# Optimization experiments

Measured on AMD Instinct MI355X. Metric: run time of the kernel, lower is better.

## Reference

```python
import jax, jax.numpy as jnp
import numpy as np

B, N, L, E = 4, 8, 2048, 16384
CH = [128, 256, 256, 256]
EPS = 1e-5
USE_MAX = True


def setup_inputs() -> dict:
    key = jax.random.key(0)
    ks = jax.random.split(key, 10)
    d = {}
    d["x"] = jax.random.normal(ks[0], (B, N, CH[0], L), jnp.float32)
    d["edge_index"] = jax.random.randint(ks[1], (2, E), 0, L, dtype=jnp.int32)
    wspecs = [("W1", CH[0], CH[1]), ("W2", CH[1], CH[2]), ("W3", CH[2], CH[3]),
              ("W1s", CH[0], CH[1]), ("W2s", CH[1], CH[2]), ("W3s", CH[2], CH[3])]
    for i, (nm, ci, co) in enumerate(wspecs):
        std = (2.0 / (ci + co)) ** 0.5  # xavier_normal
        d[nm] = std * jax.random.normal(ks[2 + i], (ci, co), jnp.float32)
        d["b" + nm[1:]] = jnp.zeros((co,), jnp.float32)
    for nm, co in [("1", CH[1]), ("2", CH[2]), ("3", CH[3]),
                   ("1s", CH[1]), ("2s", CH[2]), ("3s", CH[3])]:
        d["g" + nm] = jnp.ones((co,), jnp.float32)
        d["be" + nm] = jnp.zeros((co,), jnp.float32)
    return d


def _gcn_norm(edge_index, num_nodes):
    # PyG gcn_norm with improved=True: A_hat = A + 2I, sym normalization.
    src, dst = edge_index[0], edge_index[1]
    loop = jnp.arange(num_nodes, dtype=src.dtype)
    src = jnp.concatenate([src, loop])
    dst = jnp.concatenate([dst, loop])
    w = jnp.concatenate([jnp.ones((edge_index.shape[1],), jnp.float32),
                         jnp.full((num_nodes,), 2.0, jnp.float32)])
    deg = jnp.zeros((num_nodes,), jnp.float32).at[dst].add(w)
    dis = jnp.where(deg > 0, jax.lax.rsqrt(deg), 0.0)
    return src, dst, dis[src] * w * dis[dst]


def _gcn(h, W, bias, src, dst, norm, num_nodes):
    # h: [G, L, Cin] node features for G independent copies of the shared graph
    hw = h @ W  # [G, L, Cout]
    msgs = hw[:, src, :] * norm[None, :, None]  # gather along nodes
    agg = jnp.zeros((h.shape[0], num_nodes, W.shape[1]), h.dtype).at[:, dst].add(msgs)
    return agg + bias


def _bn(x, g, be):
    # x: [Nb, C, L]; training-mode BatchNorm1d over (Nb, L) per channel
    m = x.mean(axis=(0, 2), keepdims=True)
    v = x.var(axis=(0, 2), keepdims=True)
    return g[None, :, None] * (x - m) * jax.lax.rsqrt(v + EPS) + be[None, :, None]


def _forward(x, edge_index, params):
    b, n, c, l = x.shape
    src, dst, norm = _gcn_norm(edge_index, l)
    xo = None
    for (W, bias, Ws, bs, g, be, gs, bes) in params:
        # per-element branch
        h = x.reshape(b * n, x.shape[2], l).transpose(0, 2, 1)  # [b*n, L, C]
        x1 = _gcn(h, W, bias, src, dst, norm, l).transpose(0, 2, 1)  # [b*n, Cout, L]
        x1 = _bn(x1, g, be)
        # symmetric pooled branch
        xp = jnp.max(x, axis=1) if USE_MAX else jnp.sum(x, axis=1)  # [b, C, L]
        x2 = _gcn(xp.transpose(0, 2, 1), Ws, bs, src, dst, norm, l).transpose(0, 2, 1)
        x2 = _bn(x2, gs, bes)
        co = x2.shape[1]
        x2 = jnp.broadcast_to(x2[:, None], (b, n, co, l)).reshape(b * n, co, l)
        xo = jax.nn.relu(x1 + x2)  # [b*n, Cout, L]
        x = xo.reshape(b, n, co, l)
    return xo  # final output is [b*n, CH[3], L] (not reshaped back)


def reference(x, edge_index, W1, b1, W2, b2, W3, b3, W1s, b1s, W2s, b2s, W3s, b3s,
              g1, be1, g2, be2, g3, be3, g1s, be1s, g2s, be2s, g3s, be3s):
    params = [(W1, b1, W1s, b1s, g1, be1, g1s, be1s),
              (W2, b2, W2s, b2s, g2, be2, g2s, be2s),
              (W3, b3, W3s, b3s, g3, be3, g3s, be3s)]
    return _forward(x, edge_index, params)
```

## Files before the change

### kernel.cpp

```cpp
#include <hip/hip_runtime.h>
#include <math.h>

#define LNODES 2048
#define NEDGE 16384
#define GBIG 32
#define GSM 4
#define NCOUT 256
#define BN_EPS 1e-5f
#define ND 32

typedef unsigned short u16;
typedef __attribute__((ext_vector_type(8))) short bf16x8;
typedef __attribute__((ext_vector_type(4))) float f32x4;

__device__ __forceinline__ unsigned pk2(float a, float b) {
  unsigned ua = __float_as_uint(a); ua += 0x7fffu + ((ua >> 16) & 1u);
  unsigned ub = __float_as_uint(b); ub += 0x7fffu + ((ub >> 16) & 1u);
  return (ua >> 16) | (ub & 0xffff0000u);
}
__device__ __forceinline__ float blo(unsigned u) { return __uint_as_float(u << 16); }
__device__ __forceinline__ float bhi(unsigned u) { return __uint_as_float(u & 0xffff0000u); }

__device__ __forceinline__ void gl16(const u16* g, u16* l) {
  __builtin_amdgcn_global_load_lds(
      (const __attribute__((address_space(1))) void*)g,
      (__attribute__((address_space(3))) void*)l, 16, 0, 0);
}


struct WCvt {
  const float* src[6];
  u16* dst[6];
  int ci[6];
};

__global__ __launch_bounds__(256) void setup1_k(const int* __restrict__ ei,
                                                float* __restrict__ deg,
                                                int* __restrict__ cnt,
                                                WCvt wp,
                                                const float* __restrict__ x_in,
                                                u16* __restrict__ XT0) {
  __shared__ float T[64][65];
  const int bid = blockIdx.x;
  const int t = threadIdx.x;
  if (bid < 64) {
    int e = bid * 256 + t;
    int d = ei[NEDGE + e];
    atomicAdd(&deg[d], 1.0f);
    atomicAdd(&cnt[d], 1);
  } else if (bid < 160) {
    const int w = bid - 64;
    const int bz = w >> 4;
    const int Ci = wp.ci[bz];
    const int ci0 = ((w >> 2) & 3) * 64;
    if (ci0 >= Ci) return;
    const float* W = wp.src[bz];
    u16* WT = wp.dst[bz];
    const int co0 = (w & 3) * 64;
    const int tr = t >> 4;
    const int tc = (t & 15) * 4;
#pragma unroll
    for (int p = 0; p < 4; ++p) {
      int ci = ci0 + tr + p * 16;
      float4 v = *reinterpret_cast<const float4*>(&W[(size_t)ci * NCOUT + co0 + tc]);
      T[tr + p * 16][tc + 0] = v.x; T[tr + p * 16][tc + 1] = v.y;
      T[tr + p * 16][tc + 2] = v.z; T[tr + p * 16][tc + 3] = v.w;
    }
    __syncthreads();
    const int ci = ci0 + tc;
    const int kt = ci >> 5;
    const int kk = ci & 31;
#pragma unroll
    for (int p = 0; p < 4; ++p) {
      int co = co0 + tr + p * 16;
      uint2 o = {pk2(T[tc + 0][co - co0], T[tc + 1][co - co0]),
                 pk2(T[tc + 2][co - co0], T[tc + 3][co - co0])};
      size_t idx = (size_t)kt * 8192 + (unsigned)((co * 32 + kk) ^ ((co & 7) << 3));
      *reinterpret_cast<uint2*>(&WT[idx]) = o;
    }
  } else {
    const int w = bid - 160;
    const int g = w >> 6;
    const int n0 = (w & 31) * 64;
    const int c0 = ((w >> 5) & 1) * 64;
    const int tr = t >> 4;
    const int tc = (t & 15) * 4;
#pragma unroll
    for (int p = 0; p < 4; ++p) {
      int ci = c0 + tr + p * 16;
      float4 v = *reinterpret_cast<const float4*>(&x_in[((size_t)g * 128 + ci) * LNODES + n0 + tc]);
      T[tr + p * 16][tc + 0] = v.x; T[tr + p * 16][tc + 1] = v.y;
      T[tr + p * 16][tc + 2] = v.z; T[tr + p * 16][tc + 3] = v.w;
    }
    __syncthreads();
#pragma unroll
    for (int p = 0; p < 4; ++p) {
      int nd = tr + p * 16;
      uint2 o = {pk2(T[tc + 0][nd], T[tc + 1][nd]), pk2(T[tc + 2][nd], T[tc + 3][nd])};
      *reinterpret_cast<uint2*>(&XT0[((size_t)g * LNODES + n0 + nd) * 128 + c0 + tc]) = o;
    }
  }
}

__global__ __launch_bounds__(256) void setup2_k(const float* __restrict__ deg,
                                                float* __restrict__ dis,
                                                float* __restrict__ selfn,
                                                const int* __restrict__ cnt,
                                                int* __restrict__ rp) {
  __shared__ int part[256];
  const int t = threadIdx.x;
  if (blockIdx.x == 8) {
    int base = t * 8;
    int loc[8];
    int s = 0;
#pragma unroll
    for (int j = 0; j < 8; ++j) { loc[j] = s; s += cnt[base + j]; }
    part[t] = s;
    __syncthreads();
    for (int off = 1; off < 256; off <<= 1) {
      int v = (t >= off) ? part[t - off] : 0;
      __syncthreads();
      part[t] += v;
      __syncthreads();
    }
    int excl = (t == 0) ? 0 : part[t - 1];
#pragma unroll
    for (int j = 0; j < 8; ++j) rp[base + j] = excl + loc[j];
    if (t == 255) rp[LNODES] = part[255];
  } else {
    int i = blockIdx.x * 256 + t;
    float di = rsqrtf(deg[i] + 2.0f);
    dis[i] = di;
    selfn[i] = 2.0f * di * di;
  }
}

__global__ __launch_bounds__(256) void setup3_k(const int* __restrict__ ei,
                                                const int* __restrict__ rp,
                                                int* __restrict__ fillc,
                                                const float* __restrict__ dis,
                                                int* __restrict__ col,
                                                float* __restrict__ wn) {
  int e = blockIdx.x * 256 + threadIdx.x;
  int s = ei[e], d = ei[NEDGE + e];
  int pos = rp[d] + atomicAdd(&fillc[d], 1);
  col[pos] = s;
  wn[pos] = dis[s] * dis[d];
}

__device__ __forceinline__ void coef_ld(const float* __restrict__ st,
                                        const float* __restrict__ ga,
                                        const float* __restrict__ be,
                                        const float* __restrict__ gs,
                                        const float* __restrict__ bes,
                                        float* lk1, float* lk2, float* lcc, int t) {
  float sA = 0.f, qA = 0.f, sB = 0.f, qB = 0.f;
#pragma unroll
  for (int x = 0; x < 8; ++x) {
    sA += st[x * NCOUT + t];
    qA += st[2048 + x * NCOUT + t];
    sB += st[4096 + x * NCOUT + t];
    qB += st[6144 + x * NCOUT + t];
  }
  const float c1 = (float)(GBIG * LNODES), c2 = (float)(GSM * LNODES);
  float mA = sA / c1;
  float vA = qA / c1 - mA * mA;
  float kA = ga[t] * rsqrtf(vA + BN_EPS);
  float mB = sB / c2;
  float vB = qB / c2 - mB * mB;
  float kB = gs[t] * rsqrtf(vB + BN_EPS);
  lk1[t] = kA;
  lk2[t] = kB;
  lcc[t] = be[t] - kA * mA + bes[t] - kB * mB;
}

template <int MODE>
__global__ __launch_bounds__(256) void gemm3_k(const u16* __restrict__ B1,
                                               const u16* __restrict__ B2,
                                               const float* __restrict__ st,
                                               const float* __restrict__ ga,
                                               const float* __restrict__ be,
                                               const float* __restrict__ gs,
                                               const float* __restrict__ bes,
                                               const u16* __restrict__ WbT,
                                               const u16* __restrict__ WsT,
                                               u16* __restrict__ HW1,
                                               u16* __restrict__ hw2) {
  constexpr int Cin = (MODE == 0) ? 128 : 256;
  constexpr int NT = Cin / 32;
  constexpr int BSH = 64 * Cin;
  constexpr int EPI = 64 * 264;
  constexpr int BASE = (BSH > EPI) ? BSH : EPI;
  __shared__ __align__(16) u16 smem[BASE + 8192];
  __shared__ float lk1[NCOUT], lk2[NCOUT], lcc[NCOUT];
  u16* Wsh = smem + BASE;
  const int z = blockIdx.z;
  const bool sym = z < GSM;
  const int g = sym ? z : z - GSM;
  u16* out = sym ? hw2 : HW1;
  const int n0 = blockIdx.x * 64;
  const int t = threadIdx.x;
  const u16* Wmat = sym ? WsT : WbT;

#pragma unroll
  for (int c = 0; c < 4; ++c)
    gl16(Wmat + c * 2048 + t * 8, &Wsh[c * 2048 + t * 8]);

  constexpr int OPR = Cin / 8;
  constexpr int RPI = 256 / OPR;
  constexpr int NIT = 64 / RPI;
  const int ro = t / OPR;
  const int ch8 = (t % OPR) * 8;

  float K1[8], K2[8], CC[8];
  if constexpr (MODE == 1) {
    coef_ld(st, ga, be, gs, bes, lk1, lk2, lcc, t);
    __syncthreads();
#pragma unroll
    for (int j = 0; j < 8; ++j) { K1[j] = lk1[ch8 + j]; K2[j] = lk2[ch8 + j]; CC[j] = lcc[ch8 + j]; }
  }

#define BIDX(r, c) ((((r) * Cin) + (c)) ^ (((r) & 7) << 3))

  if constexpr (MODE == 0) {
    if (!sym) {
      const u16* src = B1 + ((size_t)g * LNODES + n0) * Cin + ch8;
#pragma unroll
      for (int it = 0; it < NIT; ++it) {
        int row = it * RPI + ro;
        uint4 v = *reinterpret_cast<const uint4*>(&src[(size_t)row * Cin]);
        *reinterpret_cast<uint4*>(&smem[BIDX(row, ch8)]) = v;
      }
    } else {
      const size_t a1b = ((size_t)(g * 8) * LNODES + n0) * Cin + ch8;
      const size_t nstep = (size_t)LNODES * Cin;
      for (int it = 0; it < NIT; ++it) {
        int row = it * RPI + ro;
        uint4 v = *reinterpret_cast<const uint4*>(&B1[a1b + (size_t)row * Cin]);
        float m0 = blo(v.x), m1 = bhi(v.x), m2 = blo(v.y), m3 = bhi(v.y);
        float m4 = blo(v.z), m5 = bhi(v.z), m6 = blo(v.w), m7 = bhi(v.w);
#pragma unroll
        for (int n = 1; n < 8; ++n) {
          uint4 a = *reinterpret_cast<const uint4*>(&B1[a1b + n * nstep + (size_t)row * Cin]);
          m0 = fmaxf(m0, blo(a.x)); m1 = fmaxf(m1, bhi(a.x));
          m2 = fmaxf(m2, blo(a.y)); m3 = fmaxf(m3, bhi(a.y));
          m4 = fmaxf(m4, blo(a.z)); m5 = fmaxf(m5, bhi(a.z));
          m6 = fmaxf(m6, blo(a.w)); m7 = fmaxf(m7, bhi(a.w));
        }
        uint4 ov = {pk2(m0, m1), pk2(m2, m3), pk2(m4, m5), pk2(m6, m7)};
        *reinterpret_cast<uint4*>(&smem[BIDX(row, ch8)]) = ov;
      }
    }
  } else if (!sym) {
    const size_t b1o = ((size_t)g * LNODES + n0) * NCOUT + ch8;
    const size_t b2o = ((size_t)(g >> 3) * LNODES + n0) * NCOUT + ch8;
#pragma unroll
    for (int it = 0; it < NIT; ++it) {
      int row = it * RPI + ro;
      uint4 a1 = *reinterpret_cast<const uint4*>(&B1[b1o + (size_t)row * NCOUT]);
      uint4 a2 = *reinterpret_cast<const uint4*>(&B2[b2o + (size_t)row * NCOUT]);
      float o0 = fmaxf(K1[0] * blo(a1.x) + K2[0] * blo(a2.x) + CC[0], 0.f);
      float o1 = fmaxf(K1[1] * bhi(a1.x) + K2[1] * bhi(a2.x) + CC[1], 0.f);
      float o2 = fmaxf(K1[2] * blo(a1.y) + K2[2] * blo(a2.y) + CC[2], 0.f);
      float o3 = fmaxf(K1[3] * bhi(a1.y) + K2[3] * bhi(a2.y) + CC[3], 0.f);
      float o4 = fmaxf(K1[4] * blo(a1.z) + K2[4] * blo(a2.z) + CC[4], 0.f);
      float o5 = fmaxf(K1[5] * bhi(a1.z) + K2[5] * bhi(a2.z) + CC[5], 0.f);
      float o6 = fmaxf(K1[6] * blo(a1.w) + K2[6] * blo(a2.w) + CC[6], 0.f);
      float o7 = fmaxf(K1[7] * bhi(a1.w) + K2[7] * bhi(a2.w) + CC[7], 0.f);
      uint4 ov = {pk2(o0, o1), pk2(o2, o3), pk2(o4, o5), pk2(o6, o7)};
      *reinterpret_cast<uint4*>(&smem[BIDX(row, ch8)]) = ov;
    }
  } else {
    const size_t b2o = ((size_t)g * LNODES + n0) * NCOUT + ch8;
    const size_t a1b = ((size_t)(g * 8) * LNODES + n0) * NCOUT + ch8;
    const size_t nstep = (size_t)LNODES * NCOUT;
    for (int it = 0; it < NIT; ++it) {
      int row = it * RPI + ro;
      uint4 a2 = *reinterpret_cast<const uint4*>(&B2[b2o + (size_t)row * NCOUT]);
      float t0 = K2[0] * blo(a2.x) + CC[0], t1 = K2[1] * bhi(a2.x) + CC[1];
      float t2 = K2[2] * blo(a2.y) + CC[2], t3 = K2[3] * bhi(a2.y) + CC[3];
      float t4 = K2[4] * blo(a2.z) + CC[4], t5 = K2[5] * bhi(a2.z) + CC[5];
      float t6 = K2[6] * blo(a2.w) + CC[6], t7 = K2[7] * bhi(a2.w) + CC[7];
      float m0 = 0.f, m1 = 0.f, m2 = 0.f, m3 = 0.f, m4 = 0.f, m5 = 0.f, m6 = 0.f, m7 = 0.f;
#pragma unroll
      for (int n = 0; n < 8; ++n) {
        uint4 a1 = *reinterpret_cast<const uint4*>(&B1[a1b + n * nstep + (size_t)row * NCOUT]);
        m0 = fmaxf(m0, K1[0] * blo(a1.x) + t0); m1 = fmaxf(m1, K1[1] * bhi(a1.x) + t1);
        m2 = fmaxf(m2, K1[2] * blo(a1.y) + t2); m3 = fmaxf(m3, K1[3] * bhi(a1.y) + t3);
        m4 = fmaxf(m4, K1[4] * blo(a1.z) + t4); m5 = fmaxf(m5, K1[5] * bhi(a1.z) + t5);
        m6 = fmaxf(m6, K1[6] * blo(a1.w) + t6); m7 = fmaxf(m7, K1[7] * bhi(a1.w) + t7);
      }
      uint4 ov = {pk2(m0, m1), pk2(m2, m3), pk2(m4, m5), pk2(m6, m7)};
      *reinterpret_cast<uint4*>(&smem[BIDX(row, ch8)]) = ov;
    }
  }

  const int wv = t >> 6;
  const int lane = t & 63;
  const int q = lane >> 4, l = lane & 15;
  f32x4 zero = {0.f, 0.f, 0.f, 0.f};
  f32x4 acc[4][4];
#pragma unroll
  for (int i = 0; i < 4; ++i)
#pragma unroll
    for (int j = 0; j < 4; ++j) acc[i][j] = zero;

#pragma unroll
  for (int kt = 0; kt < NT; ++kt) {
    __syncthreads();
    bf16x8 af[4], bx[4];
#pragma unroll
    for (int fi = 0; fi < 4; ++fi) {
      int row = wv * 64 + fi * 16 + l;
      af[fi] = *reinterpret_cast<const bf16x8*>(&Wsh[(row * 32 + q * 8) ^ ((row & 7) << 3)]);
    }
#pragma unroll
    for (int fj = 0; fj < 4; ++fj) {
      int brow = fj * 16 + l;
      bx[fj] = *reinterpret_cast<const bf16x8*>(&smem[BIDX(brow, kt * 32 + q * 8)]);
    }
    __syncthreads();
    if (kt + 1 < NT) {
      const u16* ws = Wmat + (size_t)(kt + 1) * 8192;
#pragma unroll
      for (int c = 0; c < 4; ++c)
        gl16(ws + c * 2048 + t * 8, &Wsh[c * 2048 + t * 8]);
    }
#pragma unroll
    for (int fi = 0; fi < 4; ++fi)
#pragma unroll
      for (int fj = 0; fj < 4; ++fj)
        acc[fi][fj] = __builtin_amdgcn_mfma_f32_16x16x32_bf16(af[fi], bx[fj], acc[fi][fj], 0, 0, 0);
  }
#undef BIDX

  __syncthreads();
  u16* Csh = smem;
#pragma unroll
  for (int fi = 0; fi < 4; ++fi) {
#pragma unroll
    for (int fj = 0; fj < 4; ++fj) {
      int co_l = wv * 64 + fi * 16 + q * 4;
      int nd_l = fj * 16 + l;
      uint2 pkd = {pk2(acc[fi][fj][0], acc[fi][fj][1]),
                   pk2(acc[fi][fj][2], acc[fi][fj][3])};
      *reinterpret_cast<uint2*>(&Csh[nd_l * 264 + co_l]) = pkd;
    }
  }
  __syncthreads();
#pragma unroll
  for (int p = 0; p < 8; ++p) {
    int idx = p * 256 + t;
    int nd = idx >> 5;
    int c8 = (idx & 31) * 8;
    uint4 v = *reinterpret_cast<const uint4*>(&Csh[nd * 264 + c8]);
    *reinterpret_cast<uint4*>(&out[((size_t)g * LNODES + n0 + nd) * NCOUT + c8]) = v;
  }
}

__global__ __launch_bounds__(256) void agg_comb_k(const u16* __restrict__ HW1,
                                                  const u16* __restrict__ hw2,
                                                  const int* __restrict__ col,
                                                  const float* __restrict__ wn,
                                                  const int* __restrict__ rp,
                                                  const float* __restrict__ selfn,
                                                  u16* __restrict__ AGG1,
                                                  u16* __restrict__ agg2,
                                                  float* __restrict__ st) {
  __shared__ float lsum[8][NCOUT], lsq[8][NCOUT];
  const int bid = blockIdx.x;
  const int t = threadIdx.x;
  const int wv = t >> 6;
  float* sumO;
  float* sqO;
  int shard;
  if (bid < 1024) {
    int slot = bid >> 3;
    int chunk = slot & 63;
    int g0 = (bid & 7) + 8 * (slot >> 6);
    const int d0 = chunk * ND;
    const int h = (t >> 5) & 1;
    const int ch = (t & 31) * 8;
    const u16* baseh = HW1 + (size_t)(g0 + 16 * h) * LNODES * NCOUT;
    u16* outh = AGG1 + (size_t)(g0 + 16 * h) * LNODES * NCOUT;
    float s0 = 0.f, s1 = 0.f, s2 = 0.f, s3 = 0.f, s4 = 0.f, s5 = 0.f, s6 = 0.f, s7 = 0.f;
    float q0 = 0.f, q1 = 0.f, q2 = 0.f, q3 = 0.f, q4 = 0.f, q5 = 0.f, q6 = 0.f, q7 = 0.f;
    for (int i = wv; i < ND; i += 4) {
      int d = d0 + i;
      int e0 = rp[d], e1 = rp[d + 1];
      float sw = selfn[d];
      uint4 u = *reinterpret_cast<const uint4*>(&baseh[(size_t)d * NCOUT + ch]);
      float a0 = sw * blo(u.x), a1 = sw * bhi(u.x), a2 = sw * blo(u.y), a3 = sw * bhi(u.y);
      float a4 = sw * blo(u.z), a5 = sw * bhi(u.z), a6 = sw * blo(u.w), a7 = sw * bhi(u.w);
      int e = e0;
      const int e4 = e0 + ((e1 - e0) & ~3);
      for (; e < e4; e += 4) {
        int i0 = col[e + 0], i1 = col[e + 1], i2 = col[e + 2], i3 = col[e + 3];
        float w0 = wn[e + 0], w1 = wn[e + 1], w2 = wn[e + 2], w3 = wn[e + 3];
        uint4 v0 = *reinterpret_cast<const uint4*>(&baseh[(size_t)i0 * NCOUT + ch]);
        uint4 v1 = *reinterpret_cast<const uint4*>(&baseh[(size_t)i1 * NCOUT + ch]);
        uint4 v2 = *reinterpret_cast<const uint4*>(&baseh[(size_t)i2 * NCOUT + ch]);
        uint4 v3 = *reinterpret_cast<const uint4*>(&baseh[(size_t)i3 * NCOUT + ch]);
        a0 += w0 * blo(v0.x); a1 += w0 * bhi(v0.x); a2 += w0 * blo(v0.y); a3 += w0 * bhi(v0.y);
        a4 += w0 * blo(v0.z); a5 += w0 * bhi(v0.z); a6 += w0 * blo(v0.w); a7 += w0 * bhi(v0.w);
        a0 += w1 * blo(v1.x); a1 += w1 * bhi(v1.x); a2 += w1 * blo(v1.y); a3 += w1 * bhi(v1.y);
        a4 += w1 * blo(v1.z); a5 += w1 * bhi(v1.z); a6 += w1 * blo(v1.w); a7 += w1 * bhi(v1.w);
        a0 += w2 * blo(v2.x); a1 += w2 * bhi(v2.x); a2 += w2 * blo(v2.y); a3 += w2 * bhi(v2.y);
        a4 += w2 * blo(v2.z); a5 += w2 * bhi(v2.z); a6 += w2 * blo(v2.w); a7 += w2 * bhi(v2.w);
        a0 += w3 * blo(v3.x); a1 += w3 * bhi(v3.x); a2 += w3 * blo(v3.y); a3 += w3 * bhi(v3.y);
        a4 += w3 * blo(v3.z); a5 += w3 * bhi(v3.z); a6 += w3 * blo(v3.w); a7 += w3 * bhi(v3.w);
      }
      for (; e < e1; ++e) {
        int ci = col[e];
        float w = wn[e];
        uint4 v = *reinterpret_cast<const uint4*>(&baseh[(size_t)ci * NCOUT + ch]);
        a0 += w * blo(v.x); a1 += w * bhi(v.x); a2 += w * blo(v.y); a3 += w * bhi(v.y);
        a4 += w * blo(v.z); a5 += w * bhi(v.z); a6 += w * blo(v.w); a7 += w * bhi(v.w);
      }
      uint4 o = {pk2(a0, a1), pk2(a2, a3), pk2(a4, a5), pk2(a6, a7)};
      *reinterpret_cast<uint4*>(&outh[(size_t)d * NCOUT + ch]) = o;
      s0 += a0; s1 += a1; s2 += a2; s3 += a3; s4 += a4; s5 += a5; s6 += a6; s7 += a7;
      q0 += a0 * a0; q1 += a1 * a1; q2 += a2 * a2; q3 += a3 * a3;
      q4 += a4 * a4; q5 += a5 * a5; q6 += a6 * a6; q7 += a7 * a7;
    }
    int row = wv * 2 + h;
    float4 sa = {s0, s1, s2, s3}, sb = {s4, s5, s6, s7};
    float4 qa = {q0, q1, q2, q3}, qb = {q4, q5, q6, q7};
    *reinterpret_cast<float4*>(&lsum[row][ch]) = sa;
    *reinterpret_cast<float4*>(&lsum[row][ch + 4]) = sb;
    *reinterpret_cast<float4*>(&lsq[row][ch]) = qa;
    *reinterpret_cast<float4*>(&lsq[row][ch + 4]) = qb;
    sumO = st; sqO = st + 2048; shard = (bid & 7) * NCOUT;
  } else {
    int b2 = bid - 1024;
    int g = b2 & (GSM - 1);
    int chunk = b2 >> 2;
    const int d0 = chunk * ND;
    const int lc = (t & 63) * 4;
    const u16* base = hw2 + (size_t)g * LNODES * NCOUT;
    float4 s = {0.f, 0.f, 0.f, 0.f}, qq = {0.f, 0.f, 0.f, 0.f};
    for (int i = wv; i < ND; i += 4) {
      int d = d0 + i;
      int e0 = rp[d], e1 = rp[d + 1];
      float sw = selfn[d];
      uint2 u = *reinterpret_cast<const uint2*>(&base[(size_t)d * NCOUT + lc]);
      float4 a = {sw * blo(u.x), sw * bhi(u.x), sw * blo(u.y), sw * bhi(u.y)};
      int e = e0;
      const int e4 = e0 + ((e1 - e0) & ~3);
      for (; e < e4; e += 4) {
        int i0 = col[e + 0], i1 = col[e + 1], i2 = col[e + 2], i3 = col[e + 3];
        float w0 = wn[e + 0], w1 = wn[e + 1], w2 = wn[e + 2], w3 = wn[e + 3];
        uint2 v0 = *reinterpret_cast<const uint2*>(&base[(size_t)i0 * NCOUT + lc]);
        uint2 v1 = *reinterpret_cast<const uint2*>(&base[(size_t)i1 * NCOUT + lc]);
        uint2 v2 = *reinterpret_cast<const uint2*>(&base[(size_t)i2 * NCOUT + lc]);
        uint2 v3 = *reinterpret_cast<const uint2*>(&base[(size_t)i3 * NCOUT + lc]);
        a.x += w0 * blo(v0.x); a.y += w0 * bhi(v0.x); a.z += w0 * blo(v0.y); a.w += w0 * bhi(v0.y);
        a.x += w1 * blo(v1.x); a.y += w1 * bhi(v1.x); a.z += w1 * blo(v1.y); a.w += w1 * bhi(v1.y);
        a.x += w2 * blo(v2.x); a.y += w2 * bhi(v2.x); a.z += w2 * blo(v2.y); a.w += w2 * bhi(v2.y);
        a.x += w3 * blo(v3.x); a.y += w3 * bhi(v3.x); a.z += w3 * blo(v3.y); a.w += w3 * bhi(v3.y);
      }
      for (; e < e1; ++e) {
        float w = wn[e];
        uint2 v = *reinterpret_cast<const uint2*>(&base[(size_t)col[e] * NCOUT + lc]);
        a.x += w * blo(v.x); a.y += w * bhi(v.x); a.z += w * blo(v.y); a.w += w * bhi(v.y);
      }
      uint2 o = {pk2(a.x, a.y), pk2(a.z, a.w)};
      *reinterpret_cast<uint2*>(&agg2[((size_t)g * LNODES + d) * NCOUT + lc]) = o;
      s.x += a.x; s.y += a.y; s.z += a.z; s.w += a.w;
      qq.x += a.x * a.x; qq.y += a.y * a.y; qq.z += a.z * a.z; qq.w += a.w * a.w;
    }
    *reinterpret_cast<float4*>(&lsum[wv][lc]) = s;
    *reinterpret_cast<float4*>(&lsq[wv][lc]) = qq;
    float4 z4 = {0.f, 0.f, 0.f, 0.f};
    *reinterpret_cast<float4*>(&lsum[wv + 4][lc]) = z4;
    *reinterpret_cast<float4*>(&lsq[wv + 4][lc]) = z4;
    sumO = st + 4096; sqO = st + 6144; shard = (b2 & 7) * NCOUT;
  }
  __syncthreads();
  float ts = 0.f, tq = 0.f;
#pragma unroll
  for (int r = 0; r < 8; ++r) {
    ts += lsum[r][t];
    tq += lsq[r][t];
  }
  atomicAdd(&sumO[shard + t], ts);
  atomicAdd(&sqO[shard + t], tq);
}

__global__ __launch_bounds__(256) void fuse_tr_bf_k(const u16* __restrict__ A1,
                                                    const u16* __restrict__ A2,
                                                    const float* __restrict__ st,
                                                    const float* __restrict__ ga,
                                                    const float* __restrict__ be,
                                                    const float* __restrict__ gs,
                                                    const float* __restrict__ bes,
                                                    float* __restrict__ O) {
  __shared__ float T[64][65];
  __shared__ float lk1[NCOUT], lk2[NCOUT], lcc[NCOUT];
  const int g = blockIdx.z;
  const int d0 = blockIdx.x * 64;
  const int c0 = blockIdx.y * 64;
  const int b = g >> 3;
  const int t = threadIdx.x;
  coef_ld(st, ga, be, gs, bes, lk1, lk2, lcc, t);
  __syncthreads();
  const int tr = t >> 4;
  const int tc = (t & 15) * 4;
#pragma unroll
  for (int p = 0; p < 4; ++p) {
    int d = d0 + tr + p * 16;
    uint2 a1 = *reinterpret_cast<const uint2*>(&A1[((size_t)g * LNODES + d) * NCOUT + c0 + tc]);
    uint2 a2 = *reinterpret_cast<const uint2*>(&A2[((size_t)b * LNODES + d) * NCOUT + c0 + tc]);
    int cb = c0 + tc;
    T[tr + p * 16][tc + 0] = fmaxf(lk1[cb+0] * blo(a1.x) + lk2[cb+0] * blo(a2.x) + lcc[cb+0], 0.f);
    T[tr + p * 16][tc + 1] = fmaxf(lk1[cb+1] * bhi(a1.x) + lk2[cb+1] * bhi(a2.x) + lcc[cb+1], 0.f);
    T[tr + p * 16][tc + 2] = fmaxf(lk1[cb+2] * blo(a1.y) + lk2[cb+2] * blo(a2.y) + lcc[cb+2], 0.f);
    T[tr + p * 16][tc + 3] = fmaxf(lk1[cb+3] * bhi(a1.y) + lk2[cb+3] * bhi(a2.y) + lcc[cb+3], 0.f);
  }
  __syncthreads();
#pragma unroll
  for (int p = 0; p < 4; ++p) {
    int c = tr + p * 16;
    float4 o = {T[tc + 0][c], T[tc + 1][c], T[tc + 2][c], T[tc + 3][c]};
    *reinterpret_cast<float4*>(&O[((size_t)g * NCOUT + c0 + c) * LNODES + d0 + tc]) = o;
  }
}


extern "C" void kernel_launch(void* const* d_in, const int* in_sizes, int n_in,
                              void* d_out, int out_size, void* d_ws, size_t ws_size,
                              hipStream_t stream) {
  const float* x_in = (const float*)d_in[0];
  const int* ei = (const int*)d_in[1];
  const float* W[3]   = {(const float*)d_in[2],  (const float*)d_in[4],  (const float*)d_in[6]};
  const float* Wsym[3]= {(const float*)d_in[8],  (const float*)d_in[10], (const float*)d_in[12]};
  const float* ga[3]  = {(const float*)d_in[14], (const float*)d_in[16], (const float*)d_in[18]};
  const float* be[3]  = {(const float*)d_in[15], (const float*)d_in[17], (const float*)d_in[19]};
  const float* gs[3]  = {(const float*)d_in[20], (const float*)d_in[22], (const float*)d_in[24]};
  const float* bes[3] = {(const float*)d_in[21], (const float*)d_in[23], (const float*)d_in[25]};

  const size_t EBIG = (size_t)GBIG * LNODES * NCOUT;
  const size_t ESM = (size_t)GSM * LNODES * NCOUT;
  char* p = (char*)d_ws;
  u16* XT0  = (u16*)p; p += (size_t)GBIG * LNODES * 128 * 2;
  u16* AGG1 = (u16*)p; p += EBIG * 2;
  u16* agg2 = (u16*)p; p += ESM * 2;
  u16* hw2  = (u16*)p; p += ESM * 2;
  u16* WbT[3], *WsT[3];
  for (int i = 0; i < 3; ++i) { WbT[i] = (u16*)p; p += NCOUT * NCOUT * 2; }
  for (int i = 0; i < 3; ++i) { WsT[i] = (u16*)p; p += NCOUT * NCOUT * 2; }
  int*   rp   = (int*)p;   p += 2064 * 4;
  float* dis  = (float*)p; p += LNODES * 4;
  float* selfn= (float*)p; p += LNODES * 4;
  char* zbase = p;
  float* deg  = (float*)p; p += LNODES * 4;
  int*   cnt  = (int*)p;   p += LNODES * 4;
  int*   fillc= (int*)p;   p += LNODES * 4;
  int*   col  = (int*)p;   p += (NEDGE + 8) * 4;
  float* wn   = (float*)p; p += (NEDGE + 8) * 4;
  float* stats= (float*)p; p += 3 * 4 * 2048 * 4;
  size_t zsize = (size_t)(p - zbase);

  u16* HW1 = (u16*)d_out;
  float* stL[3] = {stats, stats + 8192, stats + 16384};

  hipMemsetAsync(zbase, 0, zsize, stream);
  WCvt wc;
  for (int i = 0; i < 3; ++i) {
    wc.src[i] = W[i];     wc.dst[i] = WbT[i];     wc.ci[i] = (i == 0) ? 128 : 256;
    wc.src[3 + i] = Wsym[i]; wc.dst[3 + i] = WsT[i]; wc.ci[3 + i] = (i == 0) ? 128 : 256;
  }
  setup1_k<<<2208, 256, 0, stream>>>(ei, deg, cnt, wc, x_in, XT0);
  setup2_k<<<9, 256, 0, stream>>>(deg, dis, selfn, cnt, rp);
  setup3_k<<<64, 256, 0, stream>>>(ei, rp, fillc, dis, col, wn);

  dim3 ggrid(LNODES / 64, 1, GBIG + GSM);
  gemm3_k<0><<<ggrid, 256, 0, stream>>>(XT0, nullptr, nullptr, nullptr, nullptr, nullptr,
                                        nullptr, WbT[0], WsT[0], HW1, hw2);
  agg_comb_k<<<1280, 256, 0, stream>>>(HW1, hw2, col, wn, rp, selfn, AGG1, agg2, stL[0]);
  gemm3_k<1><<<ggrid, 256, 0, stream>>>(AGG1, agg2, stL[0], ga[0], be[0], gs[0], bes[0],
                                        WbT[1], WsT[1], HW1, hw2);
  agg_comb_k<<<1280, 256, 0, stream>>>(HW1, hw2, col, wn, rp, selfn, AGG1, agg2, stL[1]);
  gemm3_k<1><<<ggrid, 256, 0, stream>>>(AGG1, agg2, stL[1], ga[1], be[1], gs[1], bes[1],
                                        WbT[2], WsT[2], HW1, hw2);
  agg_comb_k<<<1280, 256, 0, stream>>>(HW1, hw2, col, wn, rp, selfn, AGG1, agg2, stL[2]);
  fuse_tr_bf_k<<<dim3(LNODES / 64, NCOUT / 64, GBIG), 256, 0, stream>>>(
      AGG1, agg2, stL[2], ga[2], be[2], gs[2], bes[2], (float*)d_out);
}
```

Measured before the change: 333.6 us.

## Build CSR graph normalization in one block inside setup kernel

Merges the three setup kernels into one launch. A single extra block computes degrees, the prefix-sum row pointers, the normalization factors and the CSR fill entirely in shared memory with LDS atomics. The global deg/cnt/fillc buffers go away and the memset shrinks to the stats region. This removes two kernel launches and their serialization, but the graph build now runs serially on one workgroup and may become the tail of the setup kernel.

```diff
diff --git a/kernel.cpp b/kernel.cpp
--- a/kernel.cpp
+++ b/kernel.cpp
@@ -35,21 +35,22 @@
 };
 
 __global__ __launch_bounds__(256) void setup1_k(const int* __restrict__ ei,
-                                                float* __restrict__ deg,
-                                                int* __restrict__ cnt,
                                                 WCvt wp,
                                                 const float* __restrict__ x_in,
-                                                u16* __restrict__ XT0) {
+                                                u16* __restrict__ XT0,
+                                                int* __restrict__ rp_g,
+                                                float* __restrict__ selfn_g,
+                                                int* __restrict__ col,
+                                                float* __restrict__ wn) {
   __shared__ float T[64][65];
+  __shared__ int ldeg[LNODES];
+  __shared__ int lrp[LNODES + 1];
+  __shared__ float ldis[LNODES];
+  __shared__ int part[256];
   const int bid = blockIdx.x;
   const int t = threadIdx.x;
-  if (bid < 64) {
-    int e = bid * 256 + t;
-    int d = ei[NEDGE + e];
-    atomicAdd(&deg[d], 1.0f);
-    atomicAdd(&cnt[d], 1);
-  } else if (bid < 160) {
-    const int w = bid - 64;
+  if (bid < 96) {
+    const int w = bid;
     const int bz = w >> 4;
     const int Ci = wp.ci[bz];
     const int ci0 = ((w >> 2) & 3) * 64;
@@ -78,8 +79,8 @@
       size_t idx = (size_t)kt * 8192 + (unsigned)((co * 32 + kk) ^ ((co & 7) << 3));
       *reinterpret_cast<uint2*>(&WT[idx]) = o;
     }
-  } else {
-    const int w = bid - 160;
+  } else if (bid < 2144) {
+    const int w = bid - 96;
     const int g = w >> 6;
     const int n0 = (w & 31) * 64;
     const int c0 = ((w >> 5) & 1) * 64;
@@ -99,53 +100,50 @@
       uint2 o = {pk2(T[tc + 0][nd], T[tc + 1][nd]), pk2(T[tc + 2][nd], T[tc + 3][nd])};
       *reinterpret_cast<uint2*>(&XT0[((size_t)g * LNODES + n0 + nd) * 128 + c0 + tc]) = o;
     }
-  }
-}
-
-__global__ __launch_bounds__(256) void setup2_k(const float* __restrict__ deg,
-                                                float* __restrict__ dis,
-                                                float* __restrict__ selfn,
-                                                const int* __restrict__ cnt,
-                                                int* __restrict__ rp) {
-  __shared__ int part[256];
-  const int t = threadIdx.x;
-  if (blockIdx.x == 8) {
-    int base = t * 8;
-    int loc[8];
-    int s = 0;
-#pragma unroll
-    for (int j = 0; j < 8; ++j) { loc[j] = s; s += cnt[base + j]; }
-    part[t] = s;
-    __syncthreads();
-    for (int off = 1; off < 256; off <<= 1) {
-      int v = (t >= off) ? part[t - off] : 0;
+  } else {
+    for (int i = t; i < LNODES; i += 256) ldeg[i] = 0;
+    __syncthreads();
+    for (int i = 0; i < NEDGE; i += 256) {
+      int d = ei[NEDGE + i + t];
+      atomicAdd(&ldeg[d], 1);
+    }
+    __syncthreads();
+    {
+      int base = t * 8;
+      int loc[8];
+      int s = 0;
+#pragma unroll
+      for (int j = 0; j < 8; ++j) { loc[j] = s; s += ldeg[base + j]; }
+      part[t] = s;
       __syncthreads();
-      part[t] += v;
-      __syncthreads();
-    }
-    int excl = (t == 0) ? 0 : part[t - 1];
-#pragma unroll
-    for (int j = 0; j < 8; ++j) rp[base + j] = excl + loc[j];
-    if (t == 255) rp[LNODES] = part[255];
-  } else {
-    int i = blockIdx.x * 256 + t;
-    float di = rsqrtf(deg[i] + 2.0f);
-    dis[i] = di;
-    selfn[i] = 2.0f * di * di;
-  }
-}
-
-__global__ __launch_bounds__(256) void setup3_k(const int* __restrict__ ei,
-                                                const int* __restrict__ rp,
-                                                int* __restrict__ fillc,
-                                                const float* __restrict__ dis,
-                                                int* __restrict__ col,
-                                                float* __restrict__ wn) {
-  int e = blockIdx.x * 256 + threadIdx.x;
-  int s = ei[e], d = ei[NEDGE + e];
-  int pos = rp[d] + atomicAdd(&fillc[d], 1);
-  col[pos] = s;
-  wn[pos] = dis[s] * dis[d];
+      for (int off = 1; off < 256; off <<= 1) {
+        int v = (t >= off) ? part[t - off] : 0;
+        __syncthreads();
+        part[t] += v;
+        __syncthreads();
+      }
+      int excl = (t == 0) ? 0 : part[t - 1];
+#pragma unroll
+      for (int j = 0; j < 8; ++j) lrp[base + j] = excl + loc[j];
+      if (t == 255) lrp[LNODES] = part[255];
+    }
+    for (int i = t; i < LNODES; i += 256) {
+      float di = rsqrtf((float)ldeg[i] + 2.0f);
+      ldis[i] = di;
+      selfn_g[i] = 2.0f * di * di;
+    }
+    __syncthreads();
+    for (int i = t; i <= LNODES; i += 256) rp_g[i] = lrp[i];
+    for (int i = t; i < LNODES; i += 256) ldeg[i] = 0;
+    __syncthreads();
+    for (int i = 0; i < NEDGE; i += 256) {
+      int e = i + t;
+      int s2 = ei[e], d = ei[NEDGE + e];
+      int pos = lrp[d] + atomicAdd(&ldeg[d], 1);
+      col[pos] = s2;
+      wn[pos] = ldis[s2] * ldis[d];
+    }
+  }
 }
 
 __device__ __forceinline__ void coef_ld(const float* __restrict__ st,
@@ -550,29 +548,21 @@
   for (int i = 0; i < 3; ++i) { WbT[i] = (u16*)p; p += NCOUT * NCOUT * 2; }
   for (int i = 0; i < 3; ++i) { WsT[i] = (u16*)p; p += NCOUT * NCOUT * 2; }
   int*   rp   = (int*)p;   p += 2064 * 4;
-  float* dis  = (float*)p; p += LNODES * 4;
   float* selfn= (float*)p; p += LNODES * 4;
-  char* zbase = p;
-  float* deg  = (float*)p; p += LNODES * 4;
-  int*   cnt  = (int*)p;   p += LNODES * 4;
-  int*   fillc= (int*)p;   p += LNODES * 4;
   int*   col  = (int*)p;   p += (NEDGE + 8) * 4;
   float* wn   = (float*)p; p += (NEDGE + 8) * 4;
   float* stats= (float*)p; p += 3 * 4 * 2048 * 4;
-  size_t zsize = (size_t)(p - zbase);
 
   u16* HW1 = (u16*)d_out;
   float* stL[3] = {stats, stats + 8192, stats + 16384};
 
-  hipMemsetAsync(zbase, 0, zsize, stream);
+  hipMemsetAsync(stats, 0, 3 * 4 * 2048 * 4, stream);
   WCvt wc;
   for (int i = 0; i < 3; ++i) {
     wc.src[i] = W[i];     wc.dst[i] = WbT[i];     wc.ci[i] = (i == 0) ? 128 : 256;
     wc.src[3 + i] = Wsym[i]; wc.dst[3 + i] = WsT[i]; wc.ci[3 + i] = (i == 0) ? 128 : 256;
   }
-  setup1_k<<<2208, 256, 0, stream>>>(ei, deg, cnt, wc, x_in, XT0);
-  setup2_k<<<9, 256, 0, stream>>>(deg, dis, selfn, cnt, rp);
-  setup3_k<<<64, 256, 0, stream>>>(ei, rp, fillc, dis, col, wn);
+  setup1_k<<<2145, 256, 0, stream>>>(ei, wc, x_in, XT0, rp, selfn, col, wn);
 
   dim3 ggrid(LNODES / 64, 1, GBIG + GSM);
   gemm3_k<0><<<ggrid, 256, 0, stream>>>(XT0, nullptr, nullptr, nullptr, nullptr, nullptr,
```

New measurement: 368.3 us. 10.4% more time.
